# Optimization experiments

Measured on AMD Instinct MI355X. Metric: run time of the kernel, lower is better.

Reference implementation:

```python
import jax, jax.numpy as jnp
import numpy as np

D_MODEL = 1024
H = 16
D_K = D_MODEL // H
NEG = -1.0e9


def setup_inputs() -> dict:
    key = jax.random.key(0)
    ks = jax.random.split(key, 12)
    B, S = 2, 2048
    s = 1.0 / np.sqrt(D_MODEL)
    inp = {
        "q": jax.random.normal(ks[0], (B, S, D_MODEL), jnp.float32),
        "k": jax.random.normal(ks[1], (B, S, D_MODEL), jnp.float32),
        "v": jax.random.normal(ks[2], (B, S, D_MODEL), jnp.float32),
        "mask": jnp.tril(jnp.ones((S, S), jnp.int32))[None, None, :, :],
        "wq": jax.random.normal(ks[3], (D_MODEL, D_MODEL), jnp.float32) * s,
        "bq": jax.random.normal(ks[4], (D_MODEL,), jnp.float32) * s,
        "wk": jax.random.normal(ks[5], (D_MODEL, D_MODEL), jnp.float32) * s,
        "bk": jax.random.normal(ks[6], (D_MODEL,), jnp.float32) * s,
        "wv": jax.random.normal(ks[7], (D_MODEL, D_MODEL), jnp.float32) * s,
        "bv": jax.random.normal(ks[8], (D_MODEL,), jnp.float32) * s,
        "wo": jax.random.normal(ks[9], (D_MODEL, D_MODEL), jnp.float32) * s,
        "bo": jax.random.normal(ks[10], (D_MODEL,), jnp.float32) * s,
    }
    return inp


def _split_heads(x):
    # [B,S,D] -> [B,H,S,d_k]
    B, S, _ = x.shape
    return x.reshape(B, S, H, D_K).transpose(0, 2, 1, 3)


def reference(q, k, v, mask, wq, bq, wk, bk, wv, bv, wo, bo):
    # torch Linear: y = x @ W.T + b
    query = _split_heads(q @ wq.T + bq)
    key = _split_heads(k @ wk.T + bk)
    value = _split_heads(v @ wv.T + bv)
    # scores: [B,H,S,S]
    scores = jnp.einsum("bhqd,bhkd->bhqk", query, key) / jnp.sqrt(
        jnp.asarray(D_K, query.dtype))
    scores = jnp.where(mask == 0, jnp.asarray(NEG, scores.dtype), scores)
    attn = jax.nn.softmax(scores, axis=-1)  # dropout p=0.0 -> identity
    x = jnp.einsum("bhqk,bhkd->bhqd", attn, value)
    B, _, S, _ = x.shape
    x = x.transpose(0, 2, 1, 3).reshape(B, S, D_MODEL)
    return x @ wo.T + bo
```

## Files before the change

kernel.cpp:

```cpp
#include <hip/hip_runtime.h>
#include <hip/hip_bf16.h>
#include <cstdint>
#include <cstddef>

#define BATCH 2
#define SEQ   2048
#define DM    1024
#define NH    16
#define DK    64
#define MROWS (BATCH*SEQ)

typedef __bf16 bf16;
typedef float  f32x4  __attribute__((ext_vector_type(4)));
typedef bf16   bf16x8 __attribute__((ext_vector_type(8)));
typedef bf16   bf16x4 __attribute__((ext_vector_type(4)));
typedef short  s16x4  __attribute__((ext_vector_type(4)));

#define MFMA32(a, b, c) __builtin_amdgcn_mfma_f32_16x16x32_bf16(a, b, c, 0, 0, 0)
#define MFMA1K(a, b, c) __builtin_amdgcn_mfma_f32_16x16x16bf16_1k(a, b, c, 0, 0, 0)

union HU { bf16x8 v; s16x4 h[2]; };
union PU { bf16x4 b; s16x4 s; };

__device__ __forceinline__ void llds16(const void* gc, void* l) {
    void* g = (void*)gc;
    __builtin_amdgcn_global_load_lds(
        (__attribute__((address_space(1))) uint32_t*)g,
        (__attribute__((address_space(3))) uint32_t*)l,
        16, 0, 0);
}

__global__ __launch_bounds__(256) void k_convert(
    const float* __restrict__ q, const float* __restrict__ k, const float* __restrict__ v,
    const float* __restrict__ wq, const float* __restrict__ wk, const float* __restrict__ wv,
    const float* __restrict__ wo,
    bf16* __restrict__ qb, bf16* __restrict__ kb, bf16* __restrict__ vb,
    bf16* __restrict__ wqb, bf16* __restrict__ wkb, bf16* __restrict__ wvb,
    bf16* __restrict__ wob) {
    long t = (long)blockIdx.x * blockDim.x + threadIdx.x;
    const long NQ = (long)MROWS * DM / 4;
    const long NW = (long)DM * DM / 4;
    const float* src; bf16* dst; long off;
    if (t < NQ)            { src = q;  dst = qb;  off = t; }
    else if (t < 2*NQ)     { src = k;  dst = kb;  off = t - NQ; }
    else if (t < 3*NQ)     { src = v;  dst = vb;  off = t - 2*NQ; }
    else {
        long u = t - 3*NQ;
        if (u < NW)        { src = wq; dst = wqb; off = u; }
        else if (u < 2*NW) { src = wk; dst = wkb; off = u - NW; }
        else if (u < 3*NW) { src = wv; dst = wvb; off = u - 2*NW; }
        else               { src = wo; dst = wob; off = u - 3*NW; }
    }
    f32x4 x = *(const f32x4*)(src + off * 4);
    bf16x4 y;
    y[0] = (bf16)x[0]; y[1] = (bf16)x[1]; y[2] = (bf16)x[2]; y[3] = (bf16)x[3];
    *(bf16x4*)(dst + off * 4) = y;
}

__device__ __forceinline__ void gemm_main(const bf16* __restrict__ A, const bf16* __restrict__ B,
                                          int m0, int n0, f32x4 acc[4][4]) {
    constexpr int K = DM, BK = 32;
    __shared__ bf16 sA[128 * BK];
    __shared__ bf16 sB[128 * BK];
    const int tid = threadIdx.x;
    const int l = tid & 63, w = tid >> 6;
    const int quad = l >> 4, l15 = l & 15;
    const int wm = w & 1, wn = w >> 1;

    for (int k0 = 0; k0 < K; k0 += BK) {
#pragma unroll
        for (int i = 0; i < 2; ++i) {
            int r16 = w * 32 + i * 16;
            const bf16* ga = A + (size_t)(m0 + r16 + (l >> 2)) * K + k0 + (l & 3) * 8;
            const bf16* gb = B + (size_t)(n0 + r16 + (l >> 2)) * K + k0 + (l & 3) * 8;
            llds16(ga, &sA[r16 * BK]);
            llds16(gb, &sB[r16 * BK]);
        }
        __syncthreads();

        bf16x8 af[4], bfr[4];
#pragma unroll
        for (int mi = 0; mi < 4; ++mi)
            af[mi] = *(const bf16x8*)&sA[(wm * 64 + mi * 16 + l15) * BK + quad * 8];
#pragma unroll
        for (int ni = 0; ni < 4; ++ni)
            bfr[ni] = *(const bf16x8*)&sB[(wn * 64 + ni * 16 + l15) * BK + quad * 8];
#pragma unroll
        for (int mi = 0; mi < 4; ++mi)
#pragma unroll
            for (int ni = 0; ni < 4; ++ni)
                acc[mi][ni] = MFMA32(af[mi], bfr[ni], acc[mi][ni]);
        __syncthreads();
    }
}

__global__ __launch_bounds__(256) void k_gemm_qk(
    const bf16* __restrict__ qb, const bf16* __restrict__ kb,
    const bf16* __restrict__ wqb, const bf16* __restrict__ wkb,
    const float* __restrict__ bq, const float* __restrict__ bk,
    bf16* __restrict__ Qf, bf16* __restrict__ Kf) {
    const int z = blockIdx.z;
    const bf16* A = z ? wkb : wqb;
    const bf16* B = z ? kb : qb;
    const float* bias = z ? bk : bq;
    bf16* out = z ? Kf : Qf;
    const float scale = z ? 1.0f : 0.18033688f;

    const int m0 = blockIdx.y * 128;
    const int n0 = blockIdx.x * 128;
    f32x4 acc[4][4] = {};
    gemm_main(A, B, m0, n0, acc);

    const int tid = threadIdx.x, l = tid & 63, w = tid >> 6;
    const int quad = l >> 4, l15 = l & 15;
    const int wm = w & 1, wn = w >> 1;

    float bias_rv[4][4];
#pragma unroll
    for (int mi = 0; mi < 4; ++mi)
#pragma unroll
        for (int r = 0; r < 4; ++r)
            bias_rv[mi][r] = bias[m0 + wm * 64 + mi * 16 + quad * 4 + r];

#pragma unroll
    for (int ni = 0; ni < 4; ++ni) {
        int col = n0 + wn * 64 + ni * 16 + l15;
        int b = col >> 11, s = col & 2047;
        int kb16 = s >> 4;
#pragma unroll
        for (int mi2 = 0; mi2 < 4; mi2 += 2) {
            bf16x8 pack;
#pragma unroll
            for (int half = 0; half < 2; ++half)
#pragma unroll
                for (int r = 0; r < 4; ++r) {
                    float x = (acc[mi2 + half][ni][r] + bias_rv[mi2 + half][r]) * scale;
                    pack[half * 4 + r] = (bf16)x;
                }
            int drow = m0 + wm * 64 + mi2 * 16;
            int h = (drow >> 6) & 15, p = (drow >> 5) & 1;
            size_t entry = ((size_t)((b * NH + h) * 128 + kb16)) * 2 + p;
            *(bf16x8*)(out + entry * 512 + (size_t)(quad * 16 + l15) * 8) = pack;
        }
    }
}

__global__ __launch_bounds__(256) void k_gemm_v(
    const bf16* __restrict__ vb, const bf16* __restrict__ wvb,
    const float* __restrict__ bv, bf16* __restrict__ Vf) {
    const int m0 = blockIdx.y * 128;
    const int n0 = blockIdx.x * 128;
    f32x4 acc[4][4] = {};
    gemm_main(vb, wvb, m0, n0, acc);

    const int tid = threadIdx.x, l = tid & 63, w = tid >> 6;
    const int quad = l >> 4, l15 = l & 15;
    const int wm = w & 1, wn = w >> 1;

#pragma unroll
    for (int ni = 0; ni < 4; ++ni) {
        int col = n0 + wn * 64 + ni * 16 + l15;
        int h = col >> 6, nid = (col >> 4) & 3;
        float bias_v = bv[col];
#pragma unroll
        for (int mi2 = 0; mi2 < 4; mi2 += 2) {
            bf16x8 pack;
#pragma unroll
            for (int half = 0; half < 2; ++half)
#pragma unroll
                for (int r = 0; r < 4; ++r)
                    pack[half * 4 + r] = (bf16)(acc[mi2 + half][ni][r] + bias_v);
            int row = m0 + wm * 64 + mi2 * 16;
            int b = row >> 11, sl = row & 2047;
            size_t entry = ((size_t)(b * NH + h) * 64 + (sl >> 5)) * 4 + nid;
            *(bf16x8*)(Vf + entry * 512 + (size_t)(quad * 16 + l15) * 8) = pack;
        }
    }
}

__global__ __launch_bounds__(256) void k_gemm_out(
    const bf16* __restrict__ X, const bf16* __restrict__ wob,
    const float* __restrict__ bo, float* __restrict__ out) {
    const int m0 = blockIdx.y * 128, n0 = blockIdx.x * 128;
    f32x4 acc[4][4] = {};
    gemm_main(X, wob, m0, n0, acc);

    const int tid = threadIdx.x, l = tid & 63, w = tid >> 6;
    const int quad = l >> 4, l15 = l & 15;
    const int wm = w & 1, wn = w >> 1;
#pragma unroll
    for (int mi = 0; mi < 4; ++mi)
#pragma unroll
        for (int ni = 0; ni < 4; ++ni) {
            int col = n0 + wn * 64 + ni * 16 + l15;
            float bias_v = bo[col];
            int rbase = m0 + wm * 64 + mi * 16 + quad * 4;
#pragma unroll
            for (int r = 0; r < 4; ++r)
                out[(size_t)(rbase + r) * DM + col] = acc[mi][ni][r] + bias_v;
        }
}

__global__ __launch_bounds__(128, 3) void k_flash(const bf16* __restrict__ Qf,
                                                  const bf16* __restrict__ Kf,
                                                  const bf16* __restrict__ Vf,
                                                  bf16* __restrict__ X) {
    const int bh = blockIdx.x, qt = blockIdx.y;
    const int b = bh >> 4, h = bh & 15;
    const int tid = threadIdx.x, w = tid >> 6, l = tid & 63;
    const int quad = l >> 4, l15 = l & 15;
    __shared__ bf16 xs[2][32 * 72];

    const bf16* kf = Kf + (size_t)bh * 128 * 1024;
    const bf16* vf = Vf + (size_t)bh * 64 * 4 * 512;
    const bf16* qfp = Qf + (size_t)bh * 128 * 1024;
    const int row0 = qt * 64 + w * 32;

    HU q16[2][2];
#pragma unroll
    for (int mt = 0; mt < 2; ++mt)
#pragma unroll
        for (int p = 0; p < 2; ++p)
            q16[mt][p].v = *(const bf16x8*)(qfp + ((size_t)((row0 >> 4) + mt) * 2 + p) * 512 + (size_t)l * 8);

    float ms[2] = {-1e30f, -1e30f}, ls[2] = {0.f, 0.f};
    f32x4 of[2][4] = {};

    for (int j = 0; j <= qt; ++j) {
        HU kl[4][2];
#pragma unroll
        for (int ni = 0; ni < 4; ++ni)
#pragma unroll
            for (int p = 0; p < 2; ++p)
                kl[ni][p].v = *(const bf16x8*)(kf + ((size_t)(j * 4 + ni) * 2 + p) * 512 + (size_t)l * 8);

        f32x4 sa[2][4] = {};
#pragma unroll
        for (int kc = 0; kc < 4; ++kc)
#pragma unroll
            for (int ni = 0; ni < 4; ++ni)
#pragma unroll
                for (int mt = 0; mt < 2; ++mt)
                    sa[mt][ni] = MFMA1K(kl[ni][kc >> 1].h[kc & 1], q16[mt][kc >> 1].h[kc & 1],
                                        sa[mt][ni]);

        if (j == qt) {
#pragma unroll
            for (int mt = 0; mt < 2; ++mt)
#pragma unroll
                for (int ni = 0; ni < 4; ++ni)
#pragma unroll
                    for (int r = 0; r < 4; ++r) {
                        int n = j * 64 + ni * 16 + quad * 4 + r;
                        int m = row0 + mt * 16 + l15;
                        if (n > m) sa[mt][ni][r] = -1e30f;
                    }
        }

        s16x4 pf[2][4];
#pragma unroll
        for (int mt = 0; mt < 2; ++mt) {
            float mx = sa[mt][0][0];
#pragma unroll
            for (int ni = 0; ni < 4; ++ni)
#pragma unroll
                for (int r = 0; r < 4; ++r) mx = fmaxf(mx, sa[mt][ni][r]);
            mx = fmaxf(mx, __shfl_xor(mx, 16, 64));
            mx = fmaxf(mx, __shfl_xor(mx, 32, 64));
            float mnew = fmaxf(ms[mt], mx);
            float al = __builtin_amdgcn_exp2f(ms[mt] - mnew);
            ms[mt] = mnew;
            float sum = 0.f;
#pragma unroll
            for (int ni = 0; ni < 4; ++ni) {
                PU pu;
#pragma unroll
                for (int r = 0; r < 4; ++r) {
                    float e = __builtin_amdgcn_exp2f(sa[mt][ni][r] - mnew);
                    sum += e;
                    pu.b[r] = (bf16)e;
                }
                pf[mt][ni] = pu.s;
            }
            sum += __shfl_xor(sum, 16, 64);
            sum += __shfl_xor(sum, 32, 64);
            ls[mt] = ls[mt] * al + sum;
            float ar[4];
#pragma unroll
            for (int r = 0; r < 4; ++r) ar[r] = __shfl(al, quad * 4 + r, 16);
#pragma unroll
            for (int nid = 0; nid < 4; ++nid)
#pragma unroll
                for (int r = 0; r < 4; ++r) of[mt][nid][r] *= ar[r];
        }

#pragma unroll
        for (int sp = 0; sp < 2; ++sp)
#pragma unroll
            for (int nid = 0; nid < 4; ++nid) {
                HU vl;
                vl.v = *(const bf16x8*)(vf + ((size_t)((j * 2 + sp) * 4 + nid)) * 512 + (size_t)l * 8);
#pragma unroll
                for (int mt = 0; mt < 2; ++mt) {
                    of[mt][nid] = MFMA1K(pf[mt][sp * 2 + 0], vl.h[0], of[mt][nid]);
                    of[mt][nid] = MFMA1K(pf[mt][sp * 2 + 1], vl.h[1], of[mt][nid]);
                }
            }
    }

#pragma unroll
    for (int mt = 0; mt < 2; ++mt) {
        float rv = 1.f / ls[mt];
        float rr[4];
#pragma unroll
        for (int r = 0; r < 4; ++r) rr[r] = __shfl(rv, quad * 4 + r, 16);
#pragma unroll
        for (int nid = 0; nid < 4; ++nid)
#pragma unroll
            for (int r = 0; r < 4; ++r)
                xs[w][(mt * 16 + quad * 4 + r) * 72 + nid * 16 + l15] =
                    (bf16)(of[mt][nid][r] * rr[r]);
    }
#pragma unroll
    for (int i = 0; i < 4; ++i) {
        int rowl = i * 8 + (l >> 3);
        bf16x8 vv = *(const bf16x8*)&xs[w][rowl * 72 + (l & 7) * 8];
        *(bf16x8*)(X + (size_t)(b * SEQ + row0 + rowl) * DM + h * 64 + (l & 7) * 8) = vv;
    }
}

extern "C" void kernel_launch(void* const* d_in, const int* in_sizes, int n_in,
                              void* d_out, int out_size, void* d_ws, size_t ws_size,
                              hipStream_t stream) {
    const float* q  = (const float*)d_in[0];
    const float* k  = (const float*)d_in[1];
    const float* v  = (const float*)d_in[2];
    const float* wq = (const float*)d_in[4];
    const float* bq = (const float*)d_in[5];
    const float* wk = (const float*)d_in[6];
    const float* bk = (const float*)d_in[7];
    const float* wv = (const float*)d_in[8];
    const float* bv = (const float*)d_in[9];
    const float* wo = (const float*)d_in[10];
    const float* bo = (const float*)d_in[11];
    float* out = (float*)d_out;

    uint8_t* ws = (uint8_t*)d_ws;
    const size_t SZ_ACT = (size_t)MROWS * DM * sizeof(bf16);
    const size_t SZ_W   = (size_t)DM * DM * sizeof(bf16);
    bf16* qb  = (bf16*)(ws);
    bf16* kb  = (bf16*)(ws + SZ_ACT);
    bf16* vb  = (bf16*)(ws + 2 * SZ_ACT);
    bf16* wqb = (bf16*)(ws + 3 * SZ_ACT);
    bf16* wkb = (bf16*)(ws + 3 * SZ_ACT + SZ_W);
    bf16* wvb = (bf16*)(ws + 3 * SZ_ACT + 2 * SZ_W);
    bf16* wob = (bf16*)(ws + 3 * SZ_ACT + 3 * SZ_W);
    bf16* Qf  = (bf16*)(ws + 3 * SZ_ACT + 4 * SZ_W);
    bf16* Kf  = (bf16*)(ws + 4 * SZ_ACT + 4 * SZ_W);
    bf16* Vf  = (bf16*)(ws + 5 * SZ_ACT + 4 * SZ_W);
    bf16* X   = (bf16*)(ws + 6 * SZ_ACT + 4 * SZ_W);

    {
        long total_vec4 = 3L * MROWS * DM / 4 + 4L * DM * DM / 4;
        k_convert<<<dim3((unsigned)(total_vec4 / 256)), 256, 0, stream>>>(
            q, k, v, wq, wk, wv, wo, qb, kb, vb, wqb, wkb, wvb, wob);
    }
    k_gemm_qk<<<dim3(MROWS / 128, DM / 128, 2), 256, 0, stream>>>(
        qb, kb, wqb, wkb, bq, bk, Qf, Kf);
    k_gemm_v<<<dim3(DM / 128, MROWS / 128), 256, 0, stream>>>(vb, wvb, bv, Vf);
    k_flash<<<dim3(BATCH * NH, SEQ / 64), 128, 0, stream>>>(Qf, Kf, Vf, X);
    k_gemm_out<<<dim3(DM / 128, MROWS / 128), 256, 0, stream>>>(X, wob, bo, out);
}
```

Before: 254.5 us.

## Merge QKV projections, retile output GEMM, and prefetch K/V in flash attention

Merges the Q/K and V projection GEMMs into one launch with a z=3 grid, which removes a kernel launch and lets all three fill the device together. Narrows the output-projection GEMM tile to 128x64 so it launches twice as many blocks. In the flash kernel, the longest causal query tiles are scheduled first, the next K tile is prefetched into registers, and all V fragments for a step are loaded before use. The PV MFMA operands are also swapped so the rescale and final write no longer need lane shuffles, and the occupancy hint in the launch bounds is dropped. The price is more register pressure in the flash kernel, which may lower occupancy.

```diff
diff --git a/kernel.cpp b/kernel.cpp
--- a/kernel.cpp
+++ b/kernel.cpp
@@ -94,20 +94,23 @@
     }
 }
 
-__global__ __launch_bounds__(256) void k_gemm_qk(
-    const bf16* __restrict__ qb, const bf16* __restrict__ kb,
-    const bf16* __restrict__ wqb, const bf16* __restrict__ wkb,
-    const float* __restrict__ bq, const float* __restrict__ bk,
-    bf16* __restrict__ Qf, bf16* __restrict__ Kf) {
+__global__ __launch_bounds__(256) void k_gemm_qkv(
+    const bf16* __restrict__ qb, const bf16* __restrict__ kb, const bf16* __restrict__ vb,
+    const bf16* __restrict__ wqb, const bf16* __restrict__ wkb, const bf16* __restrict__ wvb,
+    const float* __restrict__ bq, const float* __restrict__ bk, const float* __restrict__ bv,
+    bf16* __restrict__ Qf, bf16* __restrict__ Kf, bf16* __restrict__ Vf) {
     const int z = blockIdx.z;
-    const bf16* A = z ? wkb : wqb;
-    const bf16* B = z ? kb : qb;
-    const float* bias = z ? bk : bq;
-    bf16* out = z ? Kf : Qf;
-    const float scale = z ? 1.0f : 0.18033688f;
-
-    const int m0 = blockIdx.y * 128;
-    const int n0 = blockIdx.x * 128;
+    const bf16* A; const bf16* B; const float* bias;
+    int m0, n0;
+    if (z == 2) {
+        A = vb; B = wvb; bias = bv;
+        m0 = blockIdx.x * 128;
+        n0 = blockIdx.y * 128;
+    } else {
+        A = z ? wkb : wqb; B = z ? kb : qb; bias = z ? bk : bq;
+        m0 = blockIdx.y * 128;
+        n0 = blockIdx.x * 128;
+    }
     f32x4 acc[4][4] = {};
     gemm_main(A, B, m0, n0, acc);
 
@@ -115,65 +118,55 @@
     const int quad = l >> 4, l15 = l & 15;
     const int wm = w & 1, wn = w >> 1;
 
-    float bias_rv[4][4];
-#pragma unroll
-    for (int mi = 0; mi < 4; ++mi)
-#pragma unroll
-        for (int r = 0; r < 4; ++r)
-            bias_rv[mi][r] = bias[m0 + wm * 64 + mi * 16 + quad * 4 + r];
-
-#pragma unroll
-    for (int ni = 0; ni < 4; ++ni) {
-        int col = n0 + wn * 64 + ni * 16 + l15;
-        int b = col >> 11, s = col & 2047;
-        int kb16 = s >> 4;
-#pragma unroll
-        for (int mi2 = 0; mi2 < 4; mi2 += 2) {
-            bf16x8 pack;
-#pragma unroll
-            for (int half = 0; half < 2; ++half)
-#pragma unroll
-                for (int r = 0; r < 4; ++r) {
-                    float x = (acc[mi2 + half][ni][r] + bias_rv[mi2 + half][r]) * scale;
-                    pack[half * 4 + r] = (bf16)x;
-                }
-            int drow = m0 + wm * 64 + mi2 * 16;
-            int h = (drow >> 6) & 15, p = (drow >> 5) & 1;
-            size_t entry = ((size_t)((b * NH + h) * 128 + kb16)) * 2 + p;
-            *(bf16x8*)(out + entry * 512 + (size_t)(quad * 16 + l15) * 8) = pack;
-        }
-    }
-}
-
-__global__ __launch_bounds__(256) void k_gemm_v(
-    const bf16* __restrict__ vb, const bf16* __restrict__ wvb,
-    const float* __restrict__ bv, bf16* __restrict__ Vf) {
-    const int m0 = blockIdx.y * 128;
-    const int n0 = blockIdx.x * 128;
-    f32x4 acc[4][4] = {};
-    gemm_main(vb, wvb, m0, n0, acc);
-
-    const int tid = threadIdx.x, l = tid & 63, w = tid >> 6;
-    const int quad = l >> 4, l15 = l & 15;
-    const int wm = w & 1, wn = w >> 1;
-
-#pragma unroll
-    for (int ni = 0; ni < 4; ++ni) {
-        int col = n0 + wn * 64 + ni * 16 + l15;
-        int h = col >> 6, nid = (col >> 4) & 3;
-        float bias_v = bv[col];
-#pragma unroll
-        for (int mi2 = 0; mi2 < 4; mi2 += 2) {
-            bf16x8 pack;
-#pragma unroll
-            for (int half = 0; half < 2; ++half)
-#pragma unroll
-                for (int r = 0; r < 4; ++r)
-                    pack[half * 4 + r] = (bf16)(acc[mi2 + half][ni][r] + bias_v);
-            int row = m0 + wm * 64 + mi2 * 16;
-            int b = row >> 11, sl = row & 2047;
-            size_t entry = ((size_t)(b * NH + h) * 64 + (sl >> 5)) * 4 + nid;
-            *(bf16x8*)(Vf + entry * 512 + (size_t)(quad * 16 + l15) * 8) = pack;
+    if (z == 2) {
+#pragma unroll
+        for (int ni = 0; ni < 4; ++ni) {
+            int col = n0 + wn * 64 + ni * 16 + l15;
+            int h = col >> 6, nid = (col >> 4) & 3;
+            float bias_v = bias[col];
+#pragma unroll
+            for (int mi2 = 0; mi2 < 4; mi2 += 2) {
+                bf16x8 pack;
+#pragma unroll
+                for (int half = 0; half < 2; ++half)
+#pragma unroll
+                    for (int r = 0; r < 4; ++r)
+                        pack[half * 4 + r] = (bf16)(acc[mi2 + half][ni][r] + bias_v);
+                int row = m0 + wm * 64 + mi2 * 16;
+                int b = row >> 11, sl = row & 2047;
+                size_t entry = ((size_t)(b * NH + h) * 64 + (sl >> 5)) * 4 + nid;
+                *(bf16x8*)(Vf + entry * 512 + (size_t)(quad * 16 + l15) * 8) = pack;
+            }
+        }
+    } else {
+        bf16* out = z ? Kf : Qf;
+        const float scale = z ? 1.0f : 0.18033688f;
+        float bias_rv[4][4];
+#pragma unroll
+        for (int mi = 0; mi < 4; ++mi)
+#pragma unroll
+            for (int r = 0; r < 4; ++r)
+                bias_rv[mi][r] = bias[m0 + wm * 64 + mi * 16 + quad * 4 + r];
+#pragma unroll
+        for (int ni = 0; ni < 4; ++ni) {
+            int col = n0 + wn * 64 + ni * 16 + l15;
+            int b = col >> 11, s = col & 2047;
+            int kb16 = s >> 4;
+#pragma unroll
+            for (int mi2 = 0; mi2 < 4; mi2 += 2) {
+                bf16x8 pack;
+#pragma unroll
+                for (int half = 0; half < 2; ++half)
+#pragma unroll
+                    for (int r = 0; r < 4; ++r) {
+                        float x = (acc[mi2 + half][ni][r] + bias_rv[mi2 + half][r]) * scale;
+                        pack[half * 4 + r] = (bf16)x;
+                    }
+                int drow = m0 + wm * 64 + mi2 * 16;
+                int h = (drow >> 6) & 15, p = (drow >> 5) & 1;
+                size_t entry = ((size_t)((b * NH + h) * 128 + kb16)) * 2 + p;
+                *(bf16x8*)(out + entry * 512 + (size_t)(quad * 16 + l15) * 8) = pack;
+            }
         }
     }
 }
@@ -181,18 +174,49 @@
 __global__ __launch_bounds__(256) void k_gemm_out(
     const bf16* __restrict__ X, const bf16* __restrict__ wob,
     const float* __restrict__ bo, float* __restrict__ out) {
-    const int m0 = blockIdx.y * 128, n0 = blockIdx.x * 128;
-    f32x4 acc[4][4] = {};
-    gemm_main(X, wob, m0, n0, acc);
-
-    const int tid = threadIdx.x, l = tid & 63, w = tid >> 6;
+    constexpr int K = DM, BK = 32;
+    const int m0 = blockIdx.y * 128, n0 = blockIdx.x * 64;
+    __shared__ bf16 sA[128 * BK];
+    __shared__ bf16 sB[64 * BK];
+    const int tid = threadIdx.x;
+    const int l = tid & 63, w = tid >> 6;
     const int quad = l >> 4, l15 = l & 15;
     const int wm = w & 1, wn = w >> 1;
+
+    f32x4 acc[4][2] = {};
+    for (int k0 = 0; k0 < K; k0 += BK) {
+#pragma unroll
+        for (int i = 0; i < 2; ++i) {
+            int r16 = w * 32 + i * 16;
+            const bf16* ga = X + (size_t)(m0 + r16 + (l >> 2)) * K + k0 + (l & 3) * 8;
+            llds16(ga, &sA[r16 * BK]);
+        }
+        {
+            int r16 = w * 16;
+            const bf16* gb = wob + (size_t)(n0 + r16 + (l >> 2)) * K + k0 + (l & 3) * 8;
+            llds16(gb, &sB[r16 * BK]);
+        }
+        __syncthreads();
+
+        bf16x8 af[4], bfr[2];
+#pragma unroll
+        for (int mi = 0; mi < 4; ++mi)
+            af[mi] = *(const bf16x8*)&sA[(wm * 64 + mi * 16 + l15) * BK + quad * 8];
+#pragma unroll
+        for (int ni = 0; ni < 2; ++ni)
+            bfr[ni] = *(const bf16x8*)&sB[(wn * 32 + ni * 16 + l15) * BK + quad * 8];
+#pragma unroll
+        for (int mi = 0; mi < 4; ++mi)
+#pragma unroll
+            for (int ni = 0; ni < 2; ++ni)
+                acc[mi][ni] = MFMA32(af[mi], bfr[ni], acc[mi][ni]);
+        __syncthreads();
+    }
 #pragma unroll
     for (int mi = 0; mi < 4; ++mi)
 #pragma unroll
-        for (int ni = 0; ni < 4; ++ni) {
-            int col = n0 + wn * 64 + ni * 16 + l15;
+        for (int ni = 0; ni < 2; ++ni) {
+            int col = n0 + wn * 32 + ni * 16 + l15;
             float bias_v = bo[col];
             int rbase = m0 + wm * 64 + mi * 16 + quad * 4;
 #pragma unroll
@@ -201,11 +225,12 @@
         }
 }
 
-__global__ __launch_bounds__(128, 3) void k_flash(const bf16* __restrict__ Qf,
-                                                  const bf16* __restrict__ Kf,
-                                                  const bf16* __restrict__ Vf,
-                                                  bf16* __restrict__ X) {
-    const int bh = blockIdx.x, qt = blockIdx.y;
+__global__ __launch_bounds__(128) void k_flash(const bf16* __restrict__ Qf,
+                                               const bf16* __restrict__ Kf,
+                                               const bf16* __restrict__ Vf,
+                                               bf16* __restrict__ X) {
+    const int bh = blockIdx.x;
+    const int qt = 31 - blockIdx.y;
     const int b = bh >> 4, h = bh & 15;
     const int tid = threadIdx.x, w = tid >> 6, l = tid & 63;
     const int quad = l >> 4, l15 = l & 15;
@@ -226,13 +251,28 @@
     float ms[2] = {-1e30f, -1e30f}, ls[2] = {0.f, 0.f};
     f32x4 of[2][4] = {};
 
+    HU kl[4][2];
+#pragma unroll
+    for (int ni = 0; ni < 4; ++ni)
+#pragma unroll
+        for (int p = 0; p < 2; ++p)
+            kl[ni][p].v = *(const bf16x8*)(kf + ((size_t)(0 * 4 + ni) * 2 + p) * 512 + (size_t)l * 8);
+
     for (int j = 0; j <= qt; ++j) {
-        HU kl[4][2];
-#pragma unroll
-        for (int ni = 0; ni < 4; ++ni)
-#pragma unroll
-            for (int p = 0; p < 2; ++p)
-                kl[ni][p].v = *(const bf16x8*)(kf + ((size_t)(j * 4 + ni) * 2 + p) * 512 + (size_t)l * 8);
+        HU vl[2][4];
+#pragma unroll
+        for (int sp = 0; sp < 2; ++sp)
+#pragma unroll
+            for (int db = 0; db < 4; ++db)
+                vl[sp][db].v = *(const bf16x8*)(vf + ((size_t)((j * 2 + sp) * 4 + db)) * 512 + (size_t)l * 8);
+        HU kn[4][2];
+        if (j < qt) {
+#pragma unroll
+            for (int ni = 0; ni < 4; ++ni)
+#pragma unroll
+                for (int p = 0; p < 2; ++p)
+                    kn[ni][p].v = *(const bf16x8*)(kf + ((size_t)((j + 1) * 4 + ni) * 2 + p) * 512 + (size_t)l * 8);
+        }
 
         f32x4 sa[2][4] = {};
 #pragma unroll
@@ -285,41 +325,42 @@
             sum += __shfl_xor(sum, 16, 64);
             sum += __shfl_xor(sum, 32, 64);
             ls[mt] = ls[mt] * al + sum;
-            float ar[4];
-#pragma unroll
-            for (int r = 0; r < 4; ++r) ar[r] = __shfl(al, quad * 4 + r, 16);
-#pragma unroll
-            for (int nid = 0; nid < 4; ++nid)
-#pragma unroll
-                for (int r = 0; r < 4; ++r) of[mt][nid][r] *= ar[r];
+#pragma unroll
+            for (int db = 0; db < 4; ++db)
+#pragma unroll
+                for (int r = 0; r < 4; ++r) of[mt][db][r] *= al;
         }
 
 #pragma unroll
         for (int sp = 0; sp < 2; ++sp)
 #pragma unroll
-            for (int nid = 0; nid < 4; ++nid) {
-                HU vl;
-                vl.v = *(const bf16x8*)(vf + ((size_t)((j * 2 + sp) * 4 + nid)) * 512 + (size_t)l * 8);
+            for (int db = 0; db < 4; ++db)
 #pragma unroll
                 for (int mt = 0; mt < 2; ++mt) {
-                    of[mt][nid] = MFMA1K(pf[mt][sp * 2 + 0], vl.h[0], of[mt][nid]);
-                    of[mt][nid] = MFMA1K(pf[mt][sp * 2 + 1], vl.h[1], of[mt][nid]);
+                    of[mt][db] = MFMA1K(vl[sp][db].h[0], pf[mt][sp * 2 + 0], of[mt][db]);
+                    of[mt][db] = MFMA1K(vl[sp][db].h[1], pf[mt][sp * 2 + 1], of[mt][db]);
                 }
-            }
+
+        if (j < qt) {
+#pragma unroll
+            for (int ni = 0; ni < 4; ++ni)
+#pragma unroll
+                for (int p = 0; p < 2; ++p)
+                    kl[ni][p] = kn[ni][p];
+        }
     }
 
 #pragma unroll
     for (int mt = 0; mt < 2; ++mt) {
         float rv = 1.f / ls[mt];
-        float rr[4];
-#pragma unroll
-        for (int r = 0; r < 4; ++r) rr[r] = __shfl(rv, quad * 4 + r, 16);
-#pragma unroll
-        for (int nid = 0; nid < 4; ++nid)
+#pragma unroll
+        for (int db = 0; db < 4; ++db) {
+            bf16x4 pack;
 #pragma unroll
             for (int r = 0; r < 4; ++r)
-                xs[w][(mt * 16 + quad * 4 + r) * 72 + nid * 16 + l15] =
-                    (bf16)(of[mt][nid][r] * rr[r]);
+                pack[r] = (bf16)(of[mt][db][r] * rv);
+            *(bf16x4*)&xs[w][(mt * 16 + l15) * 72 + db * 16 + quad * 4] = pack;
+        }
     }
 #pragma unroll
     for (int i = 0; i < 4; ++i) {
@@ -365,9 +406,8 @@
         k_convert<<<dim3((unsigned)(total_vec4 / 256)), 256, 0, stream>>>(
             q, k, v, wq, wk, wv, wo, qb, kb, vb, wqb, wkb, wvb, wob);
     }
-    k_gemm_qk<<<dim3(MROWS / 128, DM / 128, 2), 256, 0, stream>>>(
-        qb, kb, wqb, wkb, bq, bk, Qf, Kf);
-    k_gemm_v<<<dim3(DM / 128, MROWS / 128), 256, 0, stream>>>(vb, wvb, bv, Vf);
+    k_gemm_qkv<<<dim3(32, 8, 3), 256, 0, stream>>>(
+        qb, kb, vb, wqb, wkb, wvb, bq, bk, bv, Qf, Kf, Vf);
     k_flash<<<dim3(BATCH * NH, SEQ / 64), 128, 0, stream>>>(Qf, Kf, Vf, X);
-    k_gemm_out<<<dim3(DM / 128, MROWS / 128), 256, 0, stream>>>(X, wob, bo, out);
-}
+    k_gemm_out<<<dim3(DM / 64, MROWS / 128), 256, 0, stream>>>(X, wob, bo, out);
+}
```

New measurement: 241.1 us. 1.06x faster.
